# Optimization experiments

Measured on AMD Instinct MI355X. Metric: run time of the kernel, lower is better.

Reference implementation:

```python
import jax, jax.numpy as jnp
import numpy as np

FS = 24000.0
C_SOUND = 343.0
MAX_TAU = 6
IGNORE = -100
PAIRS = np.array([(0, 1), (0, 2), (0, 3), (1, 2), (1, 3), (2, 3)])  # m1<m2 loop order
PERMS_NP = np.array([(0, 1, 2), (0, 2, 1), (1, 0, 2), (1, 2, 0), (2, 0, 1), (2, 1, 0)])  # itertools order


def _mic_locs():
    # [rad, azi_deg, ele_deg] per mic, centered at origin (matches center_mic_coords)
    coords = np.array([[0.042, 45, 35], [0.042, -45, -35], [0.042, 135, -35], [0.042, -135, 35]], dtype=np.float64)
    rad = coords[:, 0]
    azi = coords[:, 1] * 2 * np.pi / 360
    ele = coords[:, 2] * 2 * np.pi / 360
    locs = np.stack([rad * np.cos(azi) * np.cos(ele), rad * np.sin(azi) * np.cos(ele), rad * np.sin(ele)], axis=1)
    return jnp.asarray(locs, dtype=jnp.float32)

MIC_LOCS = _mic_locs()  # [4,3]


def _get_tdoa_targets(target):
    """Vectorized get_tdoa_target. target: [B,T,E,5,C].
    Assumes <=1 active class per (b,t,track) so the random class shuffle is a no-op.
    Returns (tdoas, tdoas2) as int32 [B,T,E,6]."""
    B, T, E, F, C = target.shape
    active = target[:, :, :, 0, :]                                  # [B,T,E,C] 0/1 flags
    is_active = jnp.any(active > 0, axis=-1)                        # [B,T,E]
    doa = jnp.einsum('btec,btedc->bted', active, target[:, :, :, 1:4, :])  # [B,T,E,3]
    dist = jnp.einsum('btec,btec->bte', active, target[:, :, :, 4, :])     # [B,T,E]
    src = doa * dist[..., None]                                     # [B,T,E,3]
    d = jnp.linalg.norm(src[..., None, :] - MIC_LOCS, axis=-1)      # [B,T,E,4] dist to each mic
    tdoa = d[..., PAIRS[:, 0]] - d[..., PAIRS[:, 1]]                # [B,T,E,6]
    tdoa = jnp.round(tdoa * FS / C_SOUND) + MAX_TAU                 # [B,T,E,6]
    # compact active tracks to the front (stable keeps track order, matching tr_cnt)
    order = jnp.argsort(jnp.logical_not(is_active), axis=-1)        # [B,T,E]
    gathered = jnp.take_along_axis(tdoa, order[..., None], axis=2)  # [B,T,E,6]
    n = jnp.sum(is_active, axis=-1)                                 # [B,T] number of events
    k = jnp.arange(E)[None, None, :]                                # slot index
    idx1 = jnp.clip(jnp.minimum(k, n[:, :, None] - 1), 0, E - 1)    # pad with LAST event
    idx2 = jnp.where(k < n[:, :, None], k, 0)                       # pad with FIRST event
    tdoas = jnp.take_along_axis(gathered, idx1[..., None], axis=2)
    tdoas2 = jnp.take_along_axis(gathered, idx2[..., None], axis=2)
    empty = (n == 0)[:, :, None, None]
    tdoas = jnp.where(empty, float(IGNORE), tdoas)
    tdoas2 = jnp.where(empty, float(IGNORE), tdoas2)
    return tdoas.astype(jnp.int32), tdoas2.astype(jnp.int32)


def _forward(pred, t_a, t_b):
    B, T, C, Tr, ntd = pred.shape
    N = B * T * ntd
    p = pred.transpose(0, 1, 4, 2, 3).reshape(N, C, Tr)             # [N,C,Tr]
    ta = t_a.transpose(0, 1, 3, 2).reshape(N, Tr)                   # [N,Tr]
    tb = t_b.transpose(0, 1, 3, 2).reshape(N, Tr)
    logp = jax.nn.log_softmax(p, axis=1)                            # [N,C,Tr]
    perms = jnp.asarray(PERMS_NP)                                   # [6,Tr]
    ar = jnp.arange(Tr)

    def pit(t):
        tc = jnp.clip(t, 0, C - 1)
        # L[n,i,j] = CE(pred track j, target track i); ignore_index -> 0
        L = -jnp.take_along_axis(logp, jnp.broadcast_to(tc[:, :, None], (N, Tr, Tr)), axis=1)
        L = jnp.where((t == IGNORE)[:, :, None], 0.0, L)
        pl = L[:, ar[None, :], perms].mean(axis=-1)                 # [N,6] per-perm mean loss
        pidx = jnp.argmin(pl, axis=1)                               # first min (matches torch loop)
        return jnp.take_along_axis(pl, pidx[:, None], axis=1)[:, 0], perms[pidx]

    loss1, perm1 = pit(ta)
    loss2, perm2 = pit(tb)
    use2 = loss2 < loss1                                            # torch.min keeps first on ties
    loss = jnp.where(use2, loss2, loss1)
    t_sel = jnp.where(use2[:, None], tb, ta)
    perm_sel = jnp.where(use2[:, None], perm2, perm1)

    pred_cls = jnp.argmax(p, axis=1)                                # [N,Tr]
    t_perm = jnp.take_along_axis(t_sel, perm_sel, axis=1)           # target reordered by opt perm
    valid = t_perm != IGNORE
    npred = jnp.sum(valid)
    correct = jnp.sum((pred_cls == t_perm) & valid)
    acc = jnp.where(npred > 0, correct.astype(jnp.float32) / jnp.maximum(npred, 1).astype(jnp.float32), 0.0)

    mask = loss > 0.0
    nval = jnp.sum(mask)
    lmean = jnp.where(nval > 0, jnp.sum(jnp.where(mask, loss, 0.0)) / jnp.maximum(nval, 1).astype(loss.dtype), 0.0)
    return lmean, acc


def setup_inputs() -> dict:
    key = jax.random.key(0)
    B, T, E, NCLS, NTD, CPRED = 128, 600, 3, 13, 6, 13
    k1, k2, k3, k4, k5 = jax.random.split(key, 5)
    pred = jax.random.normal(k1, (B, T, CPRED, E, NTD), dtype=jnp.float32)
    act_cls = jax.random.randint(k2, (B, T, E), 0, NCLS)
    act_flag = (jax.random.uniform(k3, (B, T, E)) < 0.5).astype(jnp.float32)
    onehot = jax.nn.one_hot(act_cls, NCLS, dtype=jnp.float32) * act_flag[..., None]  # <=1 active class/track
    doa = jax.random.normal(k4, (B, T, E, 3), dtype=jnp.float32)
    doa = doa / jnp.linalg.norm(doa, axis=-1, keepdims=True)
    dist = jax.random.uniform(k5, (B, T, E), minval=1.0, maxval=3.0, dtype=jnp.float32)
    target = jnp.concatenate([
        onehot[:, :, :, None, :],
        jnp.broadcast_to(doa[..., None], (B, T, E, 3, NCLS)),
        jnp.broadcast_to(dist[..., None, None], (B, T, E, 1, NCLS)),
    ], axis=3).astype(jnp.float32)                                  # [B,T,E,5,NCLS]
    return {"pred": pred, "target": target}


def reference(pred, target):
    t_a, t_b = _get_tdoa_targets(target)
    return _forward(pred, t_a, t_b)
```

## Files before the change

### kernel.cpp

```cpp
#include <hip/hip_runtime.h>
#include <cstdint>
#include <cstddef>

#define BT_TOTAL 76800
#define NCLS 13
#define IGN  (-100)

#define CPA   64
#define NBLKA (BT_TOTAL / CPA)
#define NF4A  (CPA * 195 / 4)
#define KA    13
#define CPB   32
#define NBLKB (BT_TOTAL / CPB)
#define ITEMS (CPB * 6)
#define NF4B  (CPB * 234 / 4)
#define KB    8

#define TGT_BYTES ((size_t)BT_TOTAL * 6 * sizeof(uint2))

struct Partial { float ls; int lc; int cor; int val; };

__device__ __forceinline__ void stage16(const float4* __restrict__ g, float4* l) {
    __builtin_amdgcn_global_load_lds((const __attribute__((address_space(1))) void*)g,
                                     (__attribute__((address_space(3))) void*)l,
                                     16, 0, 0);
}

extern "C" __global__ __launch_bounds__(256)
void tdoa_targets(const float* __restrict__ target, uint2* __restrict__ wsT) {
    const int tid = threadIdx.x;
    const int cb  = blockIdx.x * CPA;

    __shared__ float4 sA4[NF4A];
    const float* sA = (const float*)sA4;

    {
        const float4* g = (const float4*)(target + (size_t)cb * 195);
#pragma unroll
        for (int k = 0; k < KA; k++) {
            const int i = k * 256 + tid;
            if (i < NF4A) stage16(g + i, &sA4[i]);
        }
    }
    __syncthreads();

    if (tid < CPA) {
        const float* tg = sA + tid * 195;

        const float MX[4] = { 0.02432757455f,  0.02432757455f, -0.02432757455f, -0.02432757455f };
        const float MY[4] = { 0.02432757455f, -0.02432757455f,  0.02432757455f, -0.02432757455f };
        const float MZ[4] = { 0.02409021033f, -0.02409021033f, -0.02409021033f,  0.02409021033f };
        const int PI_[6] = {0,0,0,1,1,2};
        const int PJ_[6] = {1,2,3,2,3,3};

        int  td[3][6];
        bool ab[3];
        int  nact = 0;
#pragma unroll
        for (int e = 0; e < 3; e++) {
            float a[NCLS];
#pragma unroll
            for (int c = 0; c < NCLS; c++) a[c] = tg[e * 65 + c];
            bool ia = false;
#pragma unroll
            for (int c = 0; c < NCLS; c++) ia = ia || (a[c] > 0.0f);
            float d0 = 0.f, d1 = 0.f, d2 = 0.f, ds = 0.f;
#pragma unroll
            for (int c = 0; c < NCLS; c++) {
                d0 += a[c] * tg[e * 65 + 13 + c];
                d1 += a[c] * tg[e * 65 + 26 + c];
                d2 += a[c] * tg[e * 65 + 39 + c];
                ds += a[c] * tg[e * 65 + 52 + c];
            }
            const float sx = d0 * ds, sy = d1 * ds, sz = d2 * ds;
            float dm[4];
#pragma unroll
            for (int m = 0; m < 4; m++) {
                const float ex = sx - MX[m], ey = sy - MY[m], ez = sz - MZ[m];
                dm[m] = sqrtf(ex * ex + ey * ey + ez * ez);
            }
#pragma unroll
            for (int p = 0; p < 6; p++) {
                const float diff = dm[PI_[p]] - dm[PJ_[p]];
                td[e][p] = (int)rintf((diff * 24000.0f) / 343.0f) + 6;
            }
            ab[e] = ia;
            nact += ia ? 1 : 0;
        }

        const int o0 = ab[0] ? 0 : (ab[1] ? 1 : 2);
        const int o1 = (ab[0] && ab[1]) ? 1 : 2;
        const bool empty = (nact == 0);

#pragma unroll
        for (int p = 0; p < 6; p++) {
            const int g0 = (o0 == 0) ? td[0][p] : ((o0 == 1) ? td[1][p] : td[2][p]);
            const int g1 = (o1 == 1) ? td[1][p] : td[2][p];
            const int g2 = td[2][p];
            int ta0 = g0;
            int ta1 = (nact >= 2) ? g1 : g0;
            int ta2 = (nact == 3) ? g2 : ((nact == 2) ? g1 : g0);
            int tb0 = g0;
            int tb1 = (nact >= 2) ? g1 : g0;
            int tb2 = (nact == 3) ? g2 : g0;
            uint32_t w0 = (uint32_t)(ta0 & 0xff) | ((uint32_t)(ta1 & 0xff) << 8) | ((uint32_t)(ta2 & 0xff) << 16);
            uint32_t w1 = (uint32_t)(tb0 & 0xff) | ((uint32_t)(tb1 & 0xff) << 8) | ((uint32_t)(tb2 & 0xff) << 16);
            if (empty) { w0 = 0x009c9c9cu; w1 = 0x009c9c9cu; }
            wsT[(size_t)(cb + tid) * 6 + p] = make_uint2(w0, w1);
        }
    }
}

extern "C" __global__ __launch_bounds__(256)
void tdoa_loss(const float* __restrict__ pred, const uint2* __restrict__ wsT,
               Partial* __restrict__ part) {
    const int tid = threadIdx.x;
    const int cb  = blockIdx.x * CPB;

    __shared__ float4 sP4[NF4B];
    const float* sP = (const float*)sP4;

    {
        const float4* g = (const float4*)(pred + (size_t)cb * 234);
#pragma unroll
        for (int k = 0; k < KB; k++) {
            const int i = k * 256 + tid;
            if (i < NF4B) stage16(g + i, &sP4[i]);
        }
    }
    __syncthreads();

    float lsum = 0.f;
    int   lcnt = 0, cor = 0, nval = 0;

    if (tid < ITEMS) {
        const int btl = tid / 6;
        const int p   = tid - btl * 6;
        const float* pp = sP + btl * 234 + p;

        float x[NCLS][3];
#pragma unroll
        for (int c = 0; c < NCLS; c++)
#pragma unroll
            for (int j = 0; j < 3; j++)
                x[c][j] = pp[c * 18 + j * 6];

        int   am[3];
        float lse[3];
#pragma unroll
        for (int j = 0; j < 3; j++) {
            float m = x[0][j]; int a = 0;
#pragma unroll
            for (int c = 1; c < NCLS; c++) { if (x[c][j] > m) { m = x[c][j]; a = c; } }
            float s = 0.f;
#pragma unroll
            for (int c = 0; c < NCLS; c++) s += expf(x[c][j] - m);
            am[j] = a; lse[j] = m + logf(s);
        }

        const uint2 tw = wsT[(size_t)(cb + btl) * 6 + p];
        int ta[3], tb[3];
#pragma unroll
        for (int i = 0; i < 3; i++) {
            ta[i] = (int)(int8_t)(tw.x >> (8 * i));
            tb[i] = (int)(int8_t)(tw.y >> (8 * i));
        }

        float La[3][3], Lb[3][3];
#pragma unroll
        for (int i = 0; i < 3; i++) {
            const int  ca  = (ta[i] < 0) ? 0 : ta[i];
            const int  cb2 = (tb[i] < 0) ? 0 : tb[i];
            const bool ia  = (ta[i] == IGN);
            const bool ib  = (tb[i] == IGN);
#pragma unroll
            for (int j = 0; j < 3; j++) {
                La[i][j] = ia ? 0.f : (lse[j] - pp[ca  * 18 + j * 6]);
                Lb[i][j] = ib ? 0.f : (lse[j] - pp[cb2 * 18 + j * 6]);
            }
        }

        const int P0[6] = {0,0,1,1,2,2};
        const int P1[6] = {1,2,0,2,0,1};
        const int P2[6] = {2,1,2,0,1,0};
        float l1 = 0.f, l2 = 0.f; int i1 = 0, i2 = 0;
#pragma unroll
        for (int q = 0; q < 6; q++) {
            const float va = (La[0][P0[q]] + La[1][P1[q]] + La[2][P2[q]]) * (1.0f / 3.0f);
            const float vb = (Lb[0][P0[q]] + Lb[1][P1[q]] + Lb[2][P2[q]]) * (1.0f / 3.0f);
            if (q == 0) { l1 = va; l2 = vb; }
            else {
                if (va < l1) { l1 = va; i1 = q; }
                if (vb < l2) { l2 = vb; i2 = q; }
            }
        }

        const bool use2 = (l2 < l1);
        const float loss = use2 ? l2 : l1;
        const int  qsel = use2 ? i2 : i1;
        const int PK[6] = {36, 24, 33, 9, 18, 6};
        int pk = PK[0];
#pragma unroll
        for (int k = 1; k < 6; k++) pk = (qsel == k) ? PK[k] : pk;
        const int s0 = use2 ? tb[0] : ta[0];
        const int s1 = use2 ? tb[1] : ta[1];
        const int s2 = use2 ? tb[2] : ta[2];
#pragma unroll
        for (int i = 0; i < 3; i++) {
            const int pi = (pk >> (2 * i)) & 3;
            const int tp = (pi == 0) ? s0 : ((pi == 1) ? s1 : s2);
            const bool v = (tp != IGN);
            nval += v ? 1 : 0;
            cor  += (v && (am[i] == tp)) ? 1 : 0;
        }
        if (loss > 0.f) { lsum += loss; lcnt++; }
    }

#pragma unroll
    for (int off = 32; off > 0; off >>= 1) {
        lsum += __shfl_down(lsum, off, 64);
        lcnt += __shfl_down(lcnt, off, 64);
        cor  += __shfl_down(cor,  off, 64);
        nval += __shfl_down(nval, off, 64);
    }
    __shared__ float rf[4];
    __shared__ int   r1[4], r2[4], r3[4];
    const int wid = tid >> 6;
    if ((tid & 63) == 0) { rf[wid] = lsum; r1[wid] = lcnt; r2[wid] = cor; r3[wid] = nval; }
    __syncthreads();
    if (tid == 0) {
        Partial pt;
        pt.ls  = rf[0] + rf[1] + rf[2] + rf[3];
        pt.lc  = r1[0] + r1[1] + r1[2] + r1[3];
        pt.cor = r2[0] + r2[1] + r2[2] + r2[3];
        pt.val = r3[0] + r3[1] + r3[2] + r3[3];
        part[blockIdx.x] = pt;
    }
}

extern "C" __global__ __launch_bounds__(256)
void tdoa_final(const Partial* __restrict__ part, float* __restrict__ out) {
    const int tid = threadIdx.x;
    double ls = 0.0; int lc = 0, cor = 0, val = 0;
    for (int i = tid; i < NBLKB; i += 256) {
        const Partial p = part[i];
        ls += (double)p.ls; lc += p.lc; cor += p.cor; val += p.val;
    }
#pragma unroll
    for (int off = 32; off > 0; off >>= 1) {
        ls  += __shfl_down(ls,  off, 64);
        lc  += __shfl_down(lc,  off, 64);
        cor += __shfl_down(cor, off, 64);
        val += __shfl_down(val, off, 64);
    }
    __shared__ double sd[4];
    __shared__ int    s1[4], s2[4], s3[4];
    const int wid = tid >> 6;
    if ((tid & 63) == 0) { sd[wid] = ls; s1[wid] = lc; s2[wid] = cor; s3[wid] = val; }
    __syncthreads();
    if (tid == 0) {
        const double L = sd[0] + sd[1] + sd[2] + sd[3];
        const int c1 = s1[0] + s1[1] + s1[2] + s1[3];
        const int c2 = s2[0] + s2[1] + s2[2] + s2[3];
        const int c3 = s3[0] + s3[1] + s3[2] + s3[3];
        out[0] = (c1 > 0) ? (float)(L / (double)c1) : 0.0f;
        out[1] = (c3 > 0) ? ((float)c2 / (float)c3) : 0.0f;
    }
}

extern "C" void kernel_launch(void* const* d_in, const int* in_sizes, int n_in,
                              void* d_out, int out_size, void* d_ws, size_t ws_size,
                              hipStream_t stream) {
    const float* pred   = (const float*)d_in[0];
    const float* target = (const float*)d_in[1];
    uint2*   wsT  = (uint2*)d_ws;
    Partial* part = (Partial*)((char*)d_ws + TGT_BYTES);
    float* out = (float*)d_out;
    hipLaunchKernelGGL(tdoa_targets, dim3(NBLKA), dim3(256), 0, stream, target, wsT);
    hipLaunchKernelGGL(tdoa_loss,    dim3(NBLKB), dim3(256), 0, stream, pred, wsT, part);
    hipLaunchKernelGGL(tdoa_final,   dim3(1),     dim3(256), 0, stream, part, out);
}
```

Before: 161.4 us.

## Fuse TDOA target computation into loss kernel via shared memory

```diff
diff --git a/kernel.cpp b/kernel.cpp
--- a/kernel.cpp
+++ b/kernel.cpp
@@ -6,17 +6,13 @@
 #define NCLS 13
 #define IGN  (-100)
 
-#define CPA   64
-#define NBLKA (BT_TOTAL / CPA)
-#define NF4A  (CPA * 195 / 4)
-#define KA    13
 #define CPB   32
-#define NBLKB (BT_TOTAL / CPB)
+#define NBLK  (BT_TOTAL / CPB)
 #define ITEMS (CPB * 6)
-#define NF4B  (CPB * 234 / 4)
-#define KB    8
-
-#define TGT_BYTES ((size_t)BT_TOTAL * 6 * sizeof(uint2))
+#define NF4T  (CPB * 195 / 4)
+#define KT    7
+#define NF4P  (CPB * 234 / 4)
+#define KP    8
 
 struct Partial { float ls; int lc; int cor; int val; };
 
@@ -27,25 +23,35 @@
 }
 
 extern "C" __global__ __launch_bounds__(256)
-void tdoa_targets(const float* __restrict__ target, uint2* __restrict__ wsT) {
+void tdoa_fused(const float* __restrict__ pred, const float* __restrict__ target,
+                Partial* __restrict__ part) {
     const int tid = threadIdx.x;
-    const int cb  = blockIdx.x * CPA;
-
-    __shared__ float4 sA4[NF4A];
-    const float* sA = (const float*)sA4;
+    const int cb  = blockIdx.x * CPB;
+
+    __shared__ float4 sT4[NF4T];
+    __shared__ float4 sP4[NF4P];
+    __shared__ uint32_t sTd[CPB * 12];
+    const float* sTg = (const float*)sT4;
+    const float* sP  = (const float*)sP4;
 
     {
-        const float4* g = (const float4*)(target + (size_t)cb * 195);
-#pragma unroll
-        for (int k = 0; k < KA; k++) {
+        const float4* gt = (const float4*)(target + (size_t)cb * 195);
+#pragma unroll
+        for (int k = 0; k < KT; k++) {
             const int i = k * 256 + tid;
-            if (i < NF4A) stage16(g + i, &sA4[i]);
-        }
-    }
-    __syncthreads();
-
-    if (tid < CPA) {
-        const float* tg = sA + tid * 195;
+            if (i < NF4T) stage16(gt + i, &sT4[i]);
+        }
+        const float4* gp = (const float4*)(pred + (size_t)cb * 234);
+#pragma unroll
+        for (int k = 0; k < KP; k++) {
+            const int i = k * 256 + tid;
+            if (i < NF4P) stage16(gp + i, &sP4[i]);
+        }
+    }
+    __syncthreads();
+
+    if (tid < CPB) {
+        const float* tg = sTg + tid * 195;
 
         const float MX[4] = { 0.02432757455f,  0.02432757455f, -0.02432757455f, -0.02432757455f };
         const float MY[4] = { 0.02432757455f, -0.02432757455f,  0.02432757455f, -0.02432757455f };
@@ -106,26 +112,8 @@
             uint32_t w0 = (uint32_t)(ta0 & 0xff) | ((uint32_t)(ta1 & 0xff) << 8) | ((uint32_t)(ta2 & 0xff) << 16);
             uint32_t w1 = (uint32_t)(tb0 & 0xff) | ((uint32_t)(tb1 & 0xff) << 8) | ((uint32_t)(tb2 & 0xff) << 16);
             if (empty) { w0 = 0x009c9c9cu; w1 = 0x009c9c9cu; }
-            wsT[(size_t)(cb + tid) * 6 + p] = make_uint2(w0, w1);
-        }
-    }
-}
-
-extern "C" __global__ __launch_bounds__(256)
-void tdoa_loss(const float* __restrict__ pred, const uint2* __restrict__ wsT,
-               Partial* __restrict__ part) {
-    const int tid = threadIdx.x;
-    const int cb  = blockIdx.x * CPB;
-
-    __shared__ float4 sP4[NF4B];
-    const float* sP = (const float*)sP4;
-
-    {
-        const float4* g = (const float4*)(pred + (size_t)cb * 234);
-#pragma unroll
-        for (int k = 0; k < KB; k++) {
-            const int i = k * 256 + tid;
-            if (i < NF4B) stage16(g + i, &sP4[i]);
+            sTd[tid * 12 + p * 2 + 0] = w0;
+            sTd[tid * 12 + p * 2 + 1] = w1;
         }
     }
     __syncthreads();
@@ -158,12 +146,13 @@
             am[j] = a; lse[j] = m + logf(s);
         }
 
-        const uint2 tw = wsT[(size_t)(cb + btl) * 6 + p];
+        const uint32_t w0 = sTd[btl * 12 + p * 2 + 0];
+        const uint32_t w1 = sTd[btl * 12 + p * 2 + 1];
         int ta[3], tb[3];
 #pragma unroll
         for (int i = 0; i < 3; i++) {
-            ta[i] = (int)(int8_t)(tw.x >> (8 * i));
-            tb[i] = (int)(int8_t)(tw.y >> (8 * i));
+            ta[i] = (int)(int8_t)(w0 >> (8 * i));
+            tb[i] = (int)(int8_t)(w1 >> (8 * i));
         }
 
         float La[3][3], Lb[3][3];
@@ -242,7 +231,7 @@
 void tdoa_final(const Partial* __restrict__ part, float* __restrict__ out) {
     const int tid = threadIdx.x;
     double ls = 0.0; int lc = 0, cor = 0, val = 0;
-    for (int i = tid; i < NBLKB; i += 256) {
+    for (int i = tid; i < NBLK; i += 256) {
         const Partial p = part[i];
         ls += (double)p.ls; lc += p.lc; cor += p.cor; val += p.val;
     }
@@ -273,10 +262,8 @@
                               hipStream_t stream) {
     const float* pred   = (const float*)d_in[0];
     const float* target = (const float*)d_in[1];
-    uint2*   wsT  = (uint2*)d_ws;
-    Partial* part = (Partial*)((char*)d_ws + TGT_BYTES);
+    Partial* part = (Partial*)d_ws;
     float* out = (float*)d_out;
-    hipLaunchKernelGGL(tdoa_targets, dim3(NBLKA), dim3(256), 0, stream, target, wsT);
-    hipLaunchKernelGGL(tdoa_loss,    dim3(NBLKB), dim3(256), 0, stream, pred, wsT, part);
-    hipLaunchKernelGGL(tdoa_final,   dim3(1),     dim3(256), 0, stream, part, out);
-}
+    hipLaunchKernelGGL(tdoa_fused, dim3(NBLK), dim3(256), 0, stream, pred, target, part);
+    hipLaunchKernelGGL(tdoa_final, dim3(1),    dim3(256), 0, stream, part, out);
+}
```

Measured after the change: 166.4 us. 1.03x slower.

## Fuse final reduction into loss kernel via last-block atomic ticket; halve target tile

Applied to the files above, without the earlier changes.

```diff
diff --git a/kernel.cpp b/kernel.cpp
--- a/kernel.cpp
+++ b/kernel.cpp
@@ -6,10 +6,10 @@
 #define NCLS 13
 #define IGN  (-100)
 
-#define CPA   64
+#define CPA   32
 #define NBLKA (BT_TOTAL / CPA)
 #define NF4A  (CPA * 195 / 4)
-#define KA    13
+#define KA    7
 #define CPB   32
 #define NBLKB (BT_TOTAL / CPB)
 #define ITEMS (CPB * 6)
@@ -27,9 +27,12 @@
 }
 
 extern "C" __global__ __launch_bounds__(256)
-void tdoa_targets(const float* __restrict__ target, uint2* __restrict__ wsT) {
+void tdoa_targets(const float* __restrict__ target, uint2* __restrict__ wsT,
+                  int* __restrict__ counter) {
     const int tid = threadIdx.x;
     const int cb  = blockIdx.x * CPA;
+
+    if (blockIdx.x == 0 && tid == 0) *counter = 0;
 
     __shared__ float4 sA4[NF4A];
     const float* sA = (const float*)sA4;
@@ -113,7 +116,8 @@
 
 extern "C" __global__ __launch_bounds__(256)
 void tdoa_loss(const float* __restrict__ pred, const uint2* __restrict__ wsT,
-               Partial* __restrict__ part) {
+               Partial* __restrict__ part, int* __restrict__ counter,
+               float* __restrict__ out) {
     const int tid = threadIdx.x;
     const int cb  = blockIdx.x * CPB;
 
@@ -225,6 +229,7 @@
     }
     __shared__ float rf[4];
     __shared__ int   r1[4], r2[4], r3[4];
+    __shared__ int   sLast;
     const int wid = tid >> 6;
     if ((tid & 63) == 0) { rf[wid] = lsum; r1[wid] = lcnt; r2[wid] = cor; r3[wid] = nval; }
     __syncthreads();
@@ -235,36 +240,42 @@
         pt.cor = r2[0] + r2[1] + r2[2] + r2[3];
         pt.val = r3[0] + r3[1] + r3[2] + r3[3];
         part[blockIdx.x] = pt;
-    }
-}
-
-extern "C" __global__ __launch_bounds__(256)
-void tdoa_final(const Partial* __restrict__ part, float* __restrict__ out) {
-    const int tid = threadIdx.x;
-    double ls = 0.0; int lc = 0, cor = 0, val = 0;
-    for (int i = tid; i < NBLKB; i += 256) {
-        const Partial p = part[i];
-        ls += (double)p.ls; lc += p.lc; cor += p.cor; val += p.val;
-    }
-#pragma unroll
-    for (int off = 32; off > 0; off >>= 1) {
-        ls  += __shfl_down(ls,  off, 64);
-        lc  += __shfl_down(lc,  off, 64);
-        cor += __shfl_down(cor, off, 64);
-        val += __shfl_down(val, off, 64);
-    }
-    __shared__ double sd[4];
-    __shared__ int    s1[4], s2[4], s3[4];
-    const int wid = tid >> 6;
-    if ((tid & 63) == 0) { sd[wid] = ls; s1[wid] = lc; s2[wid] = cor; s3[wid] = val; }
-    __syncthreads();
-    if (tid == 0) {
-        const double L = sd[0] + sd[1] + sd[2] + sd[3];
-        const int c1 = s1[0] + s1[1] + s1[2] + s1[3];
-        const int c2 = s2[0] + s2[1] + s2[2] + s2[3];
-        const int c3 = s3[0] + s3[1] + s3[2] + s3[3];
-        out[0] = (c1 > 0) ? (float)(L / (double)c1) : 0.0f;
-        out[1] = (c3 > 0) ? ((float)c2 / (float)c3) : 0.0f;
+        __threadfence();
+        const int ticket = atomicAdd(counter, 1);
+        sLast = (ticket == NBLKB - 1) ? 1 : 0;
+    }
+    __syncthreads();
+
+    if (sLast) {
+        double ls = 0.0; int lc = 0, cr = 0, vl = 0;
+        for (int i = tid; i < NBLKB; i += 256) {
+            const uint32_t* q = (const uint32_t*)&part[i];
+            const uint32_t a0 = __hip_atomic_load(q + 0, __ATOMIC_RELAXED, __HIP_MEMORY_SCOPE_AGENT);
+            const uint32_t a1 = __hip_atomic_load(q + 1, __ATOMIC_RELAXED, __HIP_MEMORY_SCOPE_AGENT);
+            const uint32_t a2 = __hip_atomic_load(q + 2, __ATOMIC_RELAXED, __HIP_MEMORY_SCOPE_AGENT);
+            const uint32_t a3 = __hip_atomic_load(q + 3, __ATOMIC_RELAXED, __HIP_MEMORY_SCOPE_AGENT);
+            ls += (double)__uint_as_float(a0);
+            lc += (int)a1; cr += (int)a2; vl += (int)a3;
+        }
+#pragma unroll
+        for (int off = 32; off > 0; off >>= 1) {
+            ls += __shfl_down(ls, off, 64);
+            lc += __shfl_down(lc, off, 64);
+            cr += __shfl_down(cr, off, 64);
+            vl += __shfl_down(vl, off, 64);
+        }
+        __shared__ double sd[4];
+        __shared__ int    s1a[4], s2a[4], s3a[4];
+        if ((tid & 63) == 0) { sd[wid] = ls; s1a[wid] = lc; s2a[wid] = cr; s3a[wid] = vl; }
+        __syncthreads();
+        if (tid == 0) {
+            const double L = sd[0] + sd[1] + sd[2] + sd[3];
+            const int c1 = s1a[0] + s1a[1] + s1a[2] + s1a[3];
+            const int c2 = s2a[0] + s2a[1] + s2a[2] + s2a[3];
+            const int c3 = s3a[0] + s3a[1] + s3a[2] + s3a[3];
+            out[0] = (c1 > 0) ? (float)(L / (double)c1) : 0.0f;
+            out[1] = (c3 > 0) ? ((float)c2 / (float)c3) : 0.0f;
+        }
     }
 }
 
@@ -275,8 +286,8 @@
     const float* target = (const float*)d_in[1];
     uint2*   wsT  = (uint2*)d_ws;
     Partial* part = (Partial*)((char*)d_ws + TGT_BYTES);
+    int* counter  = (int*)((char*)d_ws + TGT_BYTES + (size_t)NBLKB * sizeof(Partial));
     float* out = (float*)d_out;
-    hipLaunchKernelGGL(tdoa_targets, dim3(NBLKA), dim3(256), 0, stream, target, wsT);
-    hipLaunchKernelGGL(tdoa_loss,    dim3(NBLKB), dim3(256), 0, stream, pred, wsT, part);
-    hipLaunchKernelGGL(tdoa_final,   dim3(1),     dim3(256), 0, stream, part, out);
-}
+    hipLaunchKernelGGL(tdoa_targets, dim3(NBLKA), dim3(256), 0, stream, target, wsT, counter);
+    hipLaunchKernelGGL(tdoa_loss,    dim3(NBLKB), dim3(256), 0, stream, pred, wsT, part, counter, out);
+}
```

Result: slower. 219.0 us (+35.7%).
